# Performance work log

Measured on AMD Instinct MI355X. Metric: run time of the kernel, lower is better.

Reference implementation:

```python
import jax, jax.numpy as jnp
import numpy as np

N_NODES = 50000
N_EDGES = 800000
D = 64
H = 128


def setup_inputs() -> dict:
    key = jax.random.key(0)
    ks = jax.random.split(key, 8)
    s = 0.05
    return {
        "nodes": jax.random.normal(ks[0], (N_NODES, D), jnp.float32),
        "edges": jax.random.normal(ks[1], (N_EDGES, D), jnp.float32),
        "We1": jax.random.normal(ks[2], (3 * D, H), jnp.float32) * s,
        "be1": jnp.zeros((H,), jnp.float32),
        "We2": jax.random.normal(ks[3], (H, D), jnp.float32) * s,
        "be2": jnp.zeros((D,), jnp.float32),
        "Wn1": jax.random.normal(ks[4], (2 * D, H), jnp.float32) * s,
        "bn1": jnp.zeros((H,), jnp.float32),
        "Wn2": jax.random.normal(ks[5], (H, D), jnp.float32) * s,
        "bn2": jnp.zeros((D,), jnp.float32),
        "senders": jax.random.randint(ks[6], (N_EDGES,), 0, N_NODES, jnp.int32),
        "receivers": jax.random.randint(ks[7], (N_EDGES,), 0, N_NODES, jnp.int32),
    }


def reference(nodes, edges, We1, be1, We2, be2, Wn1, bn1, Wn2, bn2, senders, receivers):
    # EdgeBlock(use_globals=False): concat[edge, receiver_node, sender_node] -> MLP
    edge_in = jnp.concatenate([edges, nodes[receivers], nodes[senders]], axis=-1)  # [E, 3D]
    h = jax.nn.relu(edge_in @ We1 + be1)
    new_edges = h @ We2 + be2  # [E, D]

    # NodeBlock(use_sent_edges=False, use_globals=False):
    # aggregate received edges via segment_sum, concat with node feats -> MLP
    agg = jax.ops.segment_sum(new_edges, receivers, num_segments=nodes.shape[0])  # [N, D]
    node_in = jnp.concatenate([agg, nodes], axis=-1)  # [N, 2D]
    h2 = jax.nn.relu(node_in @ Wn1 + bn1)
    new_nodes = h2 @ Wn2 + bn2  # [N, D]
    return new_nodes
```

## Files before the change

### kernel.cpp

```cpp
#include <hip/hip_runtime.h>

#define NN 50000
#define NE 800000

typedef __attribute__((ext_vector_type(8))) short bf16x8;
typedef __attribute__((ext_vector_type(8))) unsigned short us8;
typedef __attribute__((ext_vector_type(4))) unsigned short us4;
typedef __attribute__((ext_vector_type(4))) float f32x4;

#define MFMA16 __builtin_amdgcn_mfma_f32_16x16x32_bf16

__device__ __forceinline__ unsigned short f2b(float f) {
    union { float f; unsigned int u; } x; x.f = f;
    unsigned int r = x.u + 0x7FFFu + ((x.u >> 16) & 1u);
    return (unsigned short)(r >> 16);
}

__global__ __launch_bounds__(256) void prep_kernel(
    const float* __restrict__ nodes,
    const float* __restrict__ We1, const float* __restrict__ We2,
    const float* __restrict__ Wn1, const float* __restrict__ Wn2,
    unsigned short* __restrict__ nodes_bf,
    unsigned short* __restrict__ We1T, unsigned short* __restrict__ We2T,
    unsigned short* __restrict__ Wn1T, unsigned short* __restrict__ Wn2T)
{
    const int b = blockIdx.x, t = threadIdx.x;
    if (b < 400) {
        const float4* src = (const float4*)nodes;
        for (int i = b * 256 + t; i < NN * 16; i += 400 * 256) {
            float4 v = src[i];
            us4 o; o[0] = f2b(v.x); o[1] = f2b(v.y); o[2] = f2b(v.z); o[3] = f2b(v.w);
            *(us4*)&nodes_bf[(size_t)i * 4] = o;
        }
    } else {
        const int base = (b - 400) * 256 + t;
        for (int idx = base; idx < 57344; idx += 16 * 256) {
            if (idx < 24576) {
                int n = idx / 192, k = idx % 192;
                We1T[idx] = f2b(We1[k * 128 + n]);
            } else if (idx < 32768) {
                int j = idx - 24576; int n = j / 128, k = j % 128;
                We2T[j] = f2b(We2[k * 64 + n]);
            } else if (idx < 49152) {
                int j = idx - 32768; int n = j / 128, k = j % 128;
                Wn1T[j] = f2b(Wn1[k * 128 + n]);
            } else {
                int j = idx - 49152; int n = j / 128, k = j % 128;
                Wn2T[j] = f2b(Wn2[k * 64 + n]);
            }
        }
    }
}

__global__ __launch_bounds__(256, 4) void edge_kernel(
    const unsigned short* __restrict__ nodes_bf, const float* __restrict__ edges,
    const unsigned short* __restrict__ We1T, const float* __restrict__ be1,
    const unsigned short* __restrict__ We2T, const float* __restrict__ be2,
    const int* __restrict__ senders, const int* __restrict__ receivers,
    float* __restrict__ agg)
{
    __shared__ unsigned short xs[64 * 200];
    __shared__ unsigned short wb[128 * 40];
    __shared__ int ridx[64];
    __shared__ int sidx[64];

    const int t = threadIdx.x;
    const int e0 = blockIdx.x * 64;
    const int w = t >> 6;
    const int l = t & 63;
    const int lc = l & 15;
    const int lq = l >> 4;

    if (t < 64) { ridx[t] = receivers[e0 + t]; sidx[t] = senders[e0 + t]; }
    __syncthreads();

    #pragma unroll
    for (int i = 0; i < 4; ++i) {
        int idx = t + 256 * i;
        int m = idx >> 4, q = idx & 15;
        float4 v = *(const float4*)&edges[((size_t)(e0 + m)) * 64 + q * 4];
        us4 o; o[0] = f2b(v.x); o[1] = f2b(v.y); o[2] = f2b(v.z); o[3] = f2b(v.w);
        *(us4*)&xs[m * 200 + q * 4] = o;
    }
    #pragma unroll
    for (int i = 0; i < 2; ++i) {
        int idx = t + 256 * i;
        int m = idx >> 3, q = idx & 7;
        us8 v = *(const us8*)&nodes_bf[(size_t)ridx[m] * 64 + q * 8];
        *(us8*)&xs[m * 200 + 64 + q * 8] = v;
    }
    #pragma unroll
    for (int i = 0; i < 2; ++i) {
        int idx = t + 256 * i;
        int m = idx >> 3, q = idx & 7;
        us8 v = *(const us8*)&nodes_bf[(size_t)sidx[m] * 64 + q * 8];
        *(us8*)&xs[m * 200 + 128 + q * 8] = v;
    }
    __syncthreads();

    f32x4 acc[4][2];
    #pragma unroll
    for (int mt = 0; mt < 4; ++mt) { acc[mt][0] = (f32x4)0.f; acc[mt][1] = (f32x4)0.f; }

    for (int c = 0; c < 6; ++c) {
        const int k0 = 32 * c;
        #pragma unroll
        for (int i = 0; i < 2; ++i) {
            int idx = t + 256 * i;
            int n = idx >> 2, cc = idx & 3;
            *(us8*)&wb[n * 40 + cc * 8] = *(const us8*)&We1T[n * 192 + k0 + cc * 8];
        }
        __syncthreads();
        bf16x8 b0 = *(const bf16x8*)&wb[(w * 32 + lc) * 40 + lq * 8];
        bf16x8 b1 = *(const bf16x8*)&wb[(w * 32 + 16 + lc) * 40 + lq * 8];
        #pragma unroll
        for (int mt = 0; mt < 4; ++mt) {
            bf16x8 a = *(const bf16x8*)&xs[(mt * 16 + lc) * 200 + k0 + lq * 8];
            acc[mt][0] = MFMA16(a, b0, acc[mt][0], 0, 0, 0);
            acc[mt][1] = MFMA16(a, b1, acc[mt][1], 0, 0, 0);
        }
        __syncthreads();
    }

    #pragma unroll
    for (int nt = 0; nt < 2; ++nt) {
        int col = w * 32 + nt * 16 + lc;
        float bias = be1[col];
        #pragma unroll
        for (int mt = 0; mt < 4; ++mt) {
            #pragma unroll
            for (int r = 0; r < 4; ++r) {
                int row = mt * 16 + lq * 4 + r;
                float v = fmaxf(acc[mt][nt][r] + bias, 0.f);
                xs[row * 136 + col] = f2b(v);
            }
        }
    }
    __syncthreads();

    f32x4 acc2[4];
    #pragma unroll
    for (int mt = 0; mt < 4; ++mt) acc2[mt] = (f32x4)0.f;

    for (int c = 0; c < 4; ++c) {
        const int k0 = 32 * c;
        {
            int n = t >> 2, cc = t & 3;
            *(us8*)&wb[n * 40 + cc * 8] = *(const us8*)&We2T[n * 128 + k0 + cc * 8];
        }
        __syncthreads();
        bf16x8 b = *(const bf16x8*)&wb[(w * 16 + lc) * 40 + lq * 8];
        #pragma unroll
        for (int mt = 0; mt < 4; ++mt) {
            bf16x8 a = *(const bf16x8*)&xs[(mt * 16 + lc) * 136 + k0 + lq * 8];
            acc2[mt] = MFMA16(a, b, acc2[mt], 0, 0, 0);
        }
        __syncthreads();
    }

    const int col = w * 16 + lc;
    const float bias2 = be2[col];
    #pragma unroll
    for (int mt = 0; mt < 4; ++mt) {
        #pragma unroll
        for (int r = 0; r < 4; ++r) {
            int row = mt * 16 + lq * 4 + r;
            atomicAdd(&agg[(size_t)ridx[row] * 64 + col], acc2[mt][r] + bias2);
        }
    }
}

__global__ __launch_bounds__(256, 4) void node_kernel(
    const unsigned short* __restrict__ nodes_bf, const float* __restrict__ agg,
    const unsigned short* __restrict__ Wn1T, const float* __restrict__ bn1,
    const unsigned short* __restrict__ Wn2T, const float* __restrict__ bn2,
    float* __restrict__ out)
{
    __shared__ unsigned short xs[64 * 136];
    __shared__ unsigned short wb[128 * 40];

    const int t = threadIdx.x;
    const int n0 = blockIdx.x * 64;
    const int w = t >> 6;
    const int l = t & 63;
    const int lc = l & 15;
    const int lq = l >> 4;

    #pragma unroll
    for (int i = 0; i < 4; ++i) {
        int idx = t + 256 * i;
        int m = idx >> 4, q = idx & 15;
        int n = n0 + m;
        float4 v = make_float4(0.f, 0.f, 0.f, 0.f);
        if (n < NN) v = *(const float4*)&agg[(size_t)n * 64 + q * 4];
        us4 o; o[0] = f2b(v.x); o[1] = f2b(v.y); o[2] = f2b(v.z); o[3] = f2b(v.w);
        *(us4*)&xs[m * 136 + q * 4] = o;
    }
    #pragma unroll
    for (int i = 0; i < 2; ++i) {
        int idx = t + 256 * i;
        int m = idx >> 3, q = idx & 7;
        int n = n0 + m;
        us8 v = {0, 0, 0, 0, 0, 0, 0, 0};
        if (n < NN) v = *(const us8*)&nodes_bf[(size_t)n * 64 + q * 8];
        *(us8*)&xs[m * 136 + 64 + q * 8] = v;
    }
    __syncthreads();

    f32x4 acc[4][2];
    #pragma unroll
    for (int mt = 0; mt < 4; ++mt) { acc[mt][0] = (f32x4)0.f; acc[mt][1] = (f32x4)0.f; }

    for (int c = 0; c < 4; ++c) {
        const int k0 = 32 * c;
        #pragma unroll
        for (int i = 0; i < 2; ++i) {
            int idx = t + 256 * i;
            int n = idx >> 2, cc = idx & 3;
            *(us8*)&wb[n * 40 + cc * 8] = *(const us8*)&Wn1T[n * 128 + k0 + cc * 8];
        }
        __syncthreads();
        bf16x8 b0 = *(const bf16x8*)&wb[(w * 32 + lc) * 40 + lq * 8];
        bf16x8 b1 = *(const bf16x8*)&wb[(w * 32 + 16 + lc) * 40 + lq * 8];
        #pragma unroll
        for (int mt = 0; mt < 4; ++mt) {
            bf16x8 a = *(const bf16x8*)&xs[(mt * 16 + lc) * 136 + k0 + lq * 8];
            acc[mt][0] = MFMA16(a, b0, acc[mt][0], 0, 0, 0);
            acc[mt][1] = MFMA16(a, b1, acc[mt][1], 0, 0, 0);
        }
        __syncthreads();
    }

    #pragma unroll
    for (int nt = 0; nt < 2; ++nt) {
        int col = w * 32 + nt * 16 + lc;
        float bias = bn1[col];
        #pragma unroll
        for (int mt = 0; mt < 4; ++mt) {
            #pragma unroll
            for (int r = 0; r < 4; ++r) {
                int row = mt * 16 + lq * 4 + r;
                float v = fmaxf(acc[mt][nt][r] + bias, 0.f);
                xs[row * 136 + col] = f2b(v);
            }
        }
    }
    __syncthreads();

    f32x4 acc2[4];
    #pragma unroll
    for (int mt = 0; mt < 4; ++mt) acc2[mt] = (f32x4)0.f;

    for (int c = 0; c < 4; ++c) {
        const int k0 = 32 * c;
        {
            int n = t >> 2, cc = t & 3;
            *(us8*)&wb[n * 40 + cc * 8] = *(const us8*)&Wn2T[n * 128 + k0 + cc * 8];
        }
        __syncthreads();
        bf16x8 b = *(const bf16x8*)&wb[(w * 16 + lc) * 40 + lq * 8];
        #pragma unroll
        for (int mt = 0; mt < 4; ++mt) {
            bf16x8 a = *(const bf16x8*)&xs[(mt * 16 + lc) * 136 + k0 + lq * 8];
            acc2[mt] = MFMA16(a, b, acc2[mt], 0, 0, 0);
        }
        __syncthreads();
    }

    const int col = w * 16 + lc;
    const float bias2 = bn2[col];
    #pragma unroll
    for (int mt = 0; mt < 4; ++mt) {
        #pragma unroll
        for (int r = 0; r < 4; ++r) {
            int row = mt * 16 + lq * 4 + r;
            int n = n0 + row;
            if (n < NN) out[(size_t)n * 64 + col] = acc2[mt][r] + bias2;
        }
    }
}

extern "C" void kernel_launch(void* const* d_in, const int* in_sizes, int n_in,
                              void* d_out, int out_size, void* d_ws, size_t ws_size,
                              hipStream_t stream) {
    const float* nodes = (const float*)d_in[0];
    const float* edges = (const float*)d_in[1];
    const float* We1   = (const float*)d_in[2];
    const float* be1   = (const float*)d_in[3];
    const float* We2   = (const float*)d_in[4];
    const float* be2   = (const float*)d_in[5];
    const float* Wn1   = (const float*)d_in[6];
    const float* bn1   = (const float*)d_in[7];
    const float* Wn2   = (const float*)d_in[8];
    const float* bn2   = (const float*)d_in[9];
    const int* senders   = (const int*)d_in[10];
    const int* receivers = (const int*)d_in[11];
    float* out = (float*)d_out;

    char* ws = (char*)d_ws;
    float* agg = (float*)ws;
    unsigned short* nodes_bf = (unsigned short*)(ws + 12800000);
    unsigned short* We1T = (unsigned short*)(ws + 19200000);
    unsigned short* We2T = (unsigned short*)(ws + 19249152);
    unsigned short* Wn1T = (unsigned short*)(ws + 19265536);
    unsigned short* Wn2T = (unsigned short*)(ws + 19298304);

    hipMemsetAsync(agg, 0, (size_t)NN * 64 * sizeof(float), stream);
    prep_kernel<<<416, 256, 0, stream>>>(nodes, We1, We2, Wn1, Wn2,
                                         nodes_bf, We1T, We2T, Wn1T, Wn2T);
    edge_kernel<<<NE / 64, 256, 0, stream>>>(nodes_bf, edges, We1T, be1, We2T, be2,
                                             senders, receivers, agg);
    node_kernel<<<(NN + 63) / 64, 256, 0, stream>>>(nodes_bf, agg, Wn1T, bn1, Wn2T, bn2, out);
}
```

Measured before the change: 463.0 us.

## Accumulate edge scatter in bf16 with packed atomic adds via LDS staging

The edge kernel first stages its output tile in shared memory. It then scatters to a bf16 aggregation buffer using global_atomic_pk_add_bf16, so each atomic adds two values at once. This halves the atomic count and the memory traffic of the scatter, halves the memset size, and lets the node kernel read bf16 directly. The trade-off is precision: with about 16 edges per node on average, summing in bf16 loses accuracy and could push results past tolerance.

```diff
diff --git a/kernel.cpp b/kernel.cpp
--- a/kernel.cpp
+++ b/kernel.cpp
@@ -14,6 +14,10 @@
     union { float f; unsigned int u; } x; x.f = f;
     unsigned int r = x.u + 0x7FFFu + ((x.u >> 16) & 1u);
     return (unsigned short)(r >> 16);
+}
+
+__device__ __forceinline__ void atomic_pk_add_bf16(unsigned short* addr, unsigned int pk) {
+    asm volatile("global_atomic_pk_add_bf16 %0, %1, off" :: "v"(addr), "v"(pk) : "memory");
 }
 
 __global__ __launch_bounds__(256) void prep_kernel(
@@ -57,7 +61,7 @@
     const unsigned short* __restrict__ We1T, const float* __restrict__ be1,
     const unsigned short* __restrict__ We2T, const float* __restrict__ be2,
     const int* __restrict__ senders, const int* __restrict__ receivers,
-    float* __restrict__ agg)
+    unsigned short* __restrict__ agg_bf)
 {
     __shared__ unsigned short xs[64 * 200];
     __shared__ unsigned short wb[128 * 40];
@@ -158,20 +162,33 @@
         __syncthreads();
     }
 
-    const int col = w * 16 + lc;
-    const float bias2 = be2[col];
-    #pragma unroll
-    for (int mt = 0; mt < 4; ++mt) {
-        #pragma unroll
-        for (int r = 0; r < 4; ++r) {
-            int row = mt * 16 + lq * 4 + r;
-            atomicAdd(&agg[(size_t)ridx[row] * 64 + col], acc2[mt][r] + bias2);
-        }
+    float* fs = (float*)xs;
+    {
+        const int col = w * 16 + lc;
+        const float bias2 = be2[col];
+        #pragma unroll
+        for (int mt = 0; mt < 4; ++mt) {
+            #pragma unroll
+            for (int r = 0; r < 4; ++r) {
+                int row = mt * 16 + lq * 4 + r;
+                fs[row * 66 + col] = acc2[mt][r] + bias2;
+            }
+        }
+    }
+    __syncthreads();
+
+    #pragma unroll
+    for (int i = 0; i < 8; ++i) {
+        int p = t + 256 * i;
+        int row = p >> 5, cp = p & 31;
+        float2 v = *(const float2*)&fs[row * 66 + cp * 2];
+        unsigned int pk = (unsigned int)f2b(v.x) | ((unsigned int)f2b(v.y) << 16);
+        atomic_pk_add_bf16(&agg_bf[(size_t)ridx[row] * 64 + cp * 2], pk);
     }
 }
 
 __global__ __launch_bounds__(256, 4) void node_kernel(
-    const unsigned short* __restrict__ nodes_bf, const float* __restrict__ agg,
+    const unsigned short* __restrict__ nodes_bf, const unsigned short* __restrict__ agg_bf,
     const unsigned short* __restrict__ Wn1T, const float* __restrict__ bn1,
     const unsigned short* __restrict__ Wn2T, const float* __restrict__ bn2,
     float* __restrict__ out)
@@ -187,14 +204,13 @@
     const int lq = l >> 4;
 
     #pragma unroll
-    for (int i = 0; i < 4; ++i) {
-        int idx = t + 256 * i;
-        int m = idx >> 4, q = idx & 15;
+    for (int i = 0; i < 2; ++i) {
+        int idx = t + 256 * i;
+        int m = idx >> 3, q = idx & 7;
         int n = n0 + m;
-        float4 v = make_float4(0.f, 0.f, 0.f, 0.f);
-        if (n < NN) v = *(const float4*)&agg[(size_t)n * 64 + q * 4];
-        us4 o; o[0] = f2b(v.x); o[1] = f2b(v.y); o[2] = f2b(v.z); o[3] = f2b(v.w);
-        *(us4*)&xs[m * 136 + q * 4] = o;
+        us8 v = {0, 0, 0, 0, 0, 0, 0, 0};
+        if (n < NN) v = *(const us8*)&agg_bf[(size_t)n * 64 + q * 8];
+        *(us8*)&xs[m * 136 + q * 8] = v;
     }
     #pragma unroll
     for (int i = 0; i < 2; ++i) {
@@ -298,17 +314,17 @@
     float* out = (float*)d_out;
 
     char* ws = (char*)d_ws;
-    float* agg = (float*)ws;
+    unsigned short* agg_bf = (unsigned short*)ws;
     unsigned short* nodes_bf = (unsigned short*)(ws + 12800000);
     unsigned short* We1T = (unsigned short*)(ws + 19200000);
     unsigned short* We2T = (unsigned short*)(ws + 19249152);
     unsigned short* Wn1T = (unsigned short*)(ws + 19265536);
     unsigned short* Wn2T = (unsigned short*)(ws + 19298304);
 
-    hipMemsetAsync(agg, 0, (size_t)NN * 64 * sizeof(float), stream);
+    hipMemsetAsync(agg_bf, 0, (size_t)NN * 64 * sizeof(unsigned short), stream);
     prep_kernel<<<416, 256, 0, stream>>>(nodes, We1, We2, Wn1, Wn2,
                                          nodes_bf, We1T, We2T, Wn1T, Wn2T);
     edge_kernel<<<NE / 64, 256, 0, stream>>>(nodes_bf, edges, We1T, be1, We2T, be2,
-                                             senders, receivers, agg);
-    node_kernel<<<(NN + 63) / 64, 256, 0, stream>>>(nodes_bf, agg, Wn1T, bn1, Wn2T, bn2, out);
-}
+                                             senders, receivers, agg_bf);
+    node_kernel<<<(NN + 63) / 64, 256, 0, stream>>>(nodes_bf, agg_bf, Wn1T, bn1, Wn2T, bn2, out);
+}
```

Measured after the change: 421.2 us. -9.0%, faster.

## Bucket edges by receiver block and aggregate in shared memory

Applied to the files above, without the earlier changes.

Adds a build kernel that buckets edges by receiver group of 32 nodes, using atomic counters and a fixed-capacity list. The edge kernel then processes one bucket per block and accumulates messages with shared-memory atomics before a plain store to agg. This removes global float atomics and the agg memset. It also keeps MLP weights in registers instead of staging them through LDS per chunk. The tradeoffs are an extra pass over receivers, gathered reads of edge rows in random order, padded partial tiles, and silent truncation if a bucket exceeds 1024 edges.

```diff
diff --git a/kernel.cpp b/kernel.cpp
--- a/kernel.cpp
+++ b/kernel.cpp
@@ -2,6 +2,9 @@
 
 #define NN 50000
 #define NE 800000
+#define BK 32
+#define NB ((NN + BK - 1) / BK)
+#define MAXB 1024
 
 typedef __attribute__((ext_vector_type(8))) short bf16x8;
 typedef __attribute__((ext_vector_type(8))) unsigned short us8;
@@ -52,121 +55,153 @@
     }
 }
 
-__global__ __launch_bounds__(256, 4) void edge_kernel(
+__global__ __launch_bounds__(256) void build_kernel(
+    const int* __restrict__ receivers, int* __restrict__ gcnt, int* __restrict__ blist)
+{
+    int e = blockIdx.x * 256 + threadIdx.x;
+    if (e < NE) {
+        int r = receivers[e];
+        int b = r >> 5;
+        int pos = atomicAdd(&gcnt[b], 1);
+        if (pos < MAXB) blist[(size_t)b * MAXB + pos] = (e << 5) | (r & 31);
+    }
+}
+
+__global__ __launch_bounds__(256, 3) void edge_kernel(
     const unsigned short* __restrict__ nodes_bf, const float* __restrict__ edges,
     const unsigned short* __restrict__ We1T, const float* __restrict__ be1,
     const unsigned short* __restrict__ We2T, const float* __restrict__ be2,
-    const int* __restrict__ senders, const int* __restrict__ receivers,
-    float* __restrict__ agg)
+    const int* __restrict__ senders, const int* __restrict__ gcnt,
+    const int* __restrict__ blist, float* __restrict__ agg)
 {
     __shared__ unsigned short xs[64 * 200];
-    __shared__ unsigned short wb[128 * 40];
-    __shared__ int ridx[64];
+    __shared__ float aggs[BK * 66];
+    __shared__ int eidx[64];
+    __shared__ int lrid[64];
     __shared__ int sidx[64];
 
     const int t = threadIdx.x;
-    const int e0 = blockIdx.x * 64;
+    const int b = blockIdx.x;
+    const int n0 = b * BK;
     const int w = t >> 6;
     const int l = t & 63;
     const int lc = l & 15;
     const int lq = l >> 4;
 
-    if (t < 64) { ridx[t] = receivers[e0 + t]; sidx[t] = senders[e0 + t]; }
-    __syncthreads();
-
-    #pragma unroll
-    for (int i = 0; i < 4; ++i) {
-        int idx = t + 256 * i;
-        int m = idx >> 4, q = idx & 15;
-        float4 v = *(const float4*)&edges[((size_t)(e0 + m)) * 64 + q * 4];
-        us4 o; o[0] = f2b(v.x); o[1] = f2b(v.y); o[2] = f2b(v.z); o[3] = f2b(v.w);
-        *(us4*)&xs[m * 200 + q * 4] = o;
-    }
-    #pragma unroll
-    for (int i = 0; i < 2; ++i) {
-        int idx = t + 256 * i;
-        int m = idx >> 3, q = idx & 7;
-        us8 v = *(const us8*)&nodes_bf[(size_t)ridx[m] * 64 + q * 8];
-        *(us8*)&xs[m * 200 + 64 + q * 8] = v;
-    }
-    #pragma unroll
-    for (int i = 0; i < 2; ++i) {
-        int idx = t + 256 * i;
-        int m = idx >> 3, q = idx & 7;
-        us8 v = *(const us8*)&nodes_bf[(size_t)sidx[m] * 64 + q * 8];
-        *(us8*)&xs[m * 200 + 128 + q * 8] = v;
-    }
-    __syncthreads();
-
-    f32x4 acc[4][2];
-    #pragma unroll
-    for (int mt = 0; mt < 4; ++mt) { acc[mt][0] = (f32x4)0.f; acc[mt][1] = (f32x4)0.f; }
-
+    for (int i = t; i < BK * 66; i += 256) aggs[i] = 0.f;
+
+    bf16x8 wA0[6], wA1[6], wB[4];
+    #pragma unroll
     for (int c = 0; c < 6; ++c) {
-        const int k0 = 32 * c;
+        wA0[c] = *(const bf16x8*)&We1T[(w * 32 + lc) * 192 + c * 32 + lq * 8];
+        wA1[c] = *(const bf16x8*)&We1T[(w * 32 + 16 + lc) * 192 + c * 32 + lq * 8];
+    }
+    #pragma unroll
+    for (int c = 0; c < 4; ++c)
+        wB[c] = *(const bf16x8*)&We2T[(w * 16 + lc) * 128 + c * 32 + lq * 8];
+
+    const float b1x = be1[w * 32 + lc];
+    const float b1y = be1[w * 32 + 16 + lc];
+    const float bias2 = be2[w * 16 + lc];
+
+    int cnt = gcnt[b]; if (cnt > MAXB) cnt = MAXB;
+    const int nt = (cnt + 63) >> 6;
+
+    for (int tile = 0; tile < nt; ++tile) {
+        const int i0 = tile * 64;
+        __syncthreads();
+        if (t < 64) {
+            int i = i0 + t;
+            int e = 0, lr = -1;
+            if (i < cnt) { int pk = blist[(size_t)b * MAXB + i]; e = pk >> 5; lr = pk & 31; }
+            eidx[t] = e; lrid[t] = lr; sidx[t] = senders[e];
+        }
+        __syncthreads();
+
+        #pragma unroll
+        for (int i = 0; i < 4; ++i) {
+            int idx = t + 256 * i;
+            int m = idx >> 4, q = idx & 15;
+            float4 v = *(const float4*)&edges[(size_t)eidx[m] * 64 + q * 4];
+            us4 o; o[0] = f2b(v.x); o[1] = f2b(v.y); o[2] = f2b(v.z); o[3] = f2b(v.w);
+            *(us4*)&xs[m * 200 + q * 4] = o;
+        }
         #pragma unroll
         for (int i = 0; i < 2; ++i) {
             int idx = t + 256 * i;
-            int n = idx >> 2, cc = idx & 3;
-            *(us8*)&wb[n * 40 + cc * 8] = *(const us8*)&We1T[n * 192 + k0 + cc * 8];
-        }
-        __syncthreads();
-        bf16x8 b0 = *(const bf16x8*)&wb[(w * 32 + lc) * 40 + lq * 8];
-        bf16x8 b1 = *(const bf16x8*)&wb[(w * 32 + 16 + lc) * 40 + lq * 8];
-        #pragma unroll
-        for (int mt = 0; mt < 4; ++mt) {
-            bf16x8 a = *(const bf16x8*)&xs[(mt * 16 + lc) * 200 + k0 + lq * 8];
-            acc[mt][0] = MFMA16(a, b0, acc[mt][0], 0, 0, 0);
-            acc[mt][1] = MFMA16(a, b1, acc[mt][1], 0, 0, 0);
-        }
-        __syncthreads();
-    }
-
-    #pragma unroll
-    for (int nt = 0; nt < 2; ++nt) {
-        int col = w * 32 + nt * 16 + lc;
-        float bias = be1[col];
+            int m = idx >> 3, q = idx & 7;
+            int lr = lrid[m];
+            int rn = n0 + (lr < 0 ? 0 : lr);
+            us8 v = *(const us8*)&nodes_bf[(size_t)rn * 64 + q * 8];
+            *(us8*)&xs[m * 200 + 64 + q * 8] = v;
+        }
+        #pragma unroll
+        for (int i = 0; i < 2; ++i) {
+            int idx = t + 256 * i;
+            int m = idx >> 3, q = idx & 7;
+            us8 v = *(const us8*)&nodes_bf[(size_t)sidx[m] * 64 + q * 8];
+            *(us8*)&xs[m * 200 + 128 + q * 8] = v;
+        }
+        __syncthreads();
+
+        f32x4 acc[4][2];
+        #pragma unroll
+        for (int mt = 0; mt < 4; ++mt) { acc[mt][0] = (f32x4)0.f; acc[mt][1] = (f32x4)0.f; }
+        #pragma unroll
+        for (int c = 0; c < 6; ++c) {
+            #pragma unroll
+            for (int mt = 0; mt < 4; ++mt) {
+                bf16x8 a = *(const bf16x8*)&xs[(mt * 16 + lc) * 200 + c * 32 + lq * 8];
+                acc[mt][0] = MFMA16(a, wA0[c], acc[mt][0], 0, 0, 0);
+                acc[mt][1] = MFMA16(a, wA1[c], acc[mt][1], 0, 0, 0);
+            }
+        }
+        __syncthreads();
+
+        #pragma unroll
+        for (int nt2 = 0; nt2 < 2; ++nt2) {
+            int col = w * 32 + nt2 * 16 + lc;
+            float bias = nt2 ? b1y : b1x;
+            #pragma unroll
+            for (int mt = 0; mt < 4; ++mt) {
+                #pragma unroll
+                for (int r = 0; r < 4; ++r) {
+                    int row = mt * 16 + lq * 4 + r;
+                    float v = fmaxf(acc[mt][nt2][r] + bias, 0.f);
+                    xs[row * 136 + col] = f2b(v);
+                }
+            }
+        }
+        __syncthreads();
+
+        f32x4 acc2[4];
+        #pragma unroll
+        for (int mt = 0; mt < 4; ++mt) acc2[mt] = (f32x4)0.f;
+        #pragma unroll
+        for (int c = 0; c < 4; ++c) {
+            #pragma unroll
+            for (int mt = 0; mt < 4; ++mt) {
+                bf16x8 a = *(const bf16x8*)&xs[(mt * 16 + lc) * 136 + c * 32 + lq * 8];
+                acc2[mt] = MFMA16(a, wB[c], acc2[mt], 0, 0, 0);
+            }
+        }
+
         #pragma unroll
         for (int mt = 0; mt < 4; ++mt) {
             #pragma unroll
             for (int r = 0; r < 4; ++r) {
                 int row = mt * 16 + lq * 4 + r;
-                float v = fmaxf(acc[mt][nt][r] + bias, 0.f);
-                xs[row * 136 + col] = f2b(v);
-            }
-        }
-    }
+                int lr = lrid[row];
+                if (lr >= 0) atomicAdd(&aggs[lr * 66 + w * 16 + lc], acc2[mt][r] + bias2);
+            }
+        }
+    }
+
     __syncthreads();
-
-    f32x4 acc2[4];
-    #pragma unroll
-    for (int mt = 0; mt < 4; ++mt) acc2[mt] = (f32x4)0.f;
-
-    for (int c = 0; c < 4; ++c) {
-        const int k0 = 32 * c;
-        {
-            int n = t >> 2, cc = t & 3;
-            *(us8*)&wb[n * 40 + cc * 8] = *(const us8*)&We2T[n * 128 + k0 + cc * 8];
-        }
-        __syncthreads();
-        bf16x8 b = *(const bf16x8*)&wb[(w * 16 + lc) * 40 + lq * 8];
-        #pragma unroll
-        for (int mt = 0; mt < 4; ++mt) {
-            bf16x8 a = *(const bf16x8*)&xs[(mt * 16 + lc) * 136 + k0 + lq * 8];
-            acc2[mt] = MFMA16(a, b, acc2[mt], 0, 0, 0);
-        }
-        __syncthreads();
-    }
-
-    const int col = w * 16 + lc;
-    const float bias2 = be2[col];
-    #pragma unroll
-    for (int mt = 0; mt < 4; ++mt) {
-        #pragma unroll
-        for (int r = 0; r < 4; ++r) {
-            int row = mt * 16 + lq * 4 + r;
-            atomicAdd(&agg[(size_t)ridx[row] * 64 + col], acc2[mt][r] + bias2);
-        }
+    for (int i = t; i < BK * 64; i += 256) {
+        int row = i >> 6, c = i & 63;
+        int n = n0 + row;
+        if (n < NN) agg[(size_t)n * 64 + c] = aggs[row * 66 + c];
     }
 }
 
@@ -304,11 +339,14 @@
     unsigned short* We2T = (unsigned short*)(ws + 19249152);
     unsigned short* Wn1T = (unsigned short*)(ws + 19265536);
     unsigned short* Wn2T = (unsigned short*)(ws + 19298304);
-
-    hipMemsetAsync(agg, 0, (size_t)NN * 64 * sizeof(float), stream);
+    int* blist = (int*)(ws + 19314688);
+    int* gcnt  = (int*)(ws + 25716736);
+
+    hipMemsetAsync(gcnt, 0, NB * sizeof(int), stream);
     prep_kernel<<<416, 256, 0, stream>>>(nodes, We1, We2, Wn1, Wn2,
                                          nodes_bf, We1T, We2T, Wn1T, Wn2T);
-    edge_kernel<<<NE / 64, 256, 0, stream>>>(nodes_bf, edges, We1T, be1, We2T, be2,
-                                             senders, receivers, agg);
+    build_kernel<<<(NE + 255) / 256, 256, 0, stream>>>(receivers, gcnt, blist);
+    edge_kernel<<<NB, 256, 0, stream>>>(nodes_bf, edges, We1T, be1, We2T, be2,
+                                        senders, gcnt, blist, agg);
     node_kernel<<<(NN + 63) / 64, 256, 0, stream>>>(nodes_bf, agg, Wn1T, bn1, Wn2T, bn2, out);
 }
```

Result: slower. 753.8 us (+62.8%).
